# Kernel optimization log

Measured on AMD Instinct MI355X. Metric: run time of the kernel, lower is better.

The kernel has to match this reference:

```python
import jax, jax.numpy as jnp
import numpy as np

EPS = 1e-3       # module eps for mask normalization
LN_EPS = 1e-5    # torch LayerNorm default eps


def _layernorm(x, w, b):
    mu = jnp.mean(x, axis=-1, keepdims=True)
    var = jnp.var(x, axis=-1, keepdims=True)
    return (x - mu) * jax.lax.rsqrt(var + LN_EPS) * w + b


def setup_inputs() -> dict:
    key = jax.random.key(0)
    ks = jax.random.split(key, 8)
    N_seq, N_res, c_m, c_h, c_z = 256, 256, 256, 32, 128
    m = jax.random.normal(ks[0], (N_seq, N_res, c_m), jnp.float32)
    mask = jnp.ones((N_seq, N_res), jnp.float32)
    s_m = 1.0 / np.sqrt(c_m)
    ln_w = jnp.ones((c_m,), jnp.float32)
    ln_b = jnp.zeros((c_m,), jnp.float32)
    w1 = jax.random.normal(ks[1], (c_m, c_h), jnp.float32) * s_m
    b1 = jnp.zeros((c_h,), jnp.float32)
    w2 = jax.random.normal(ks[2], (c_m, c_h), jnp.float32) * s_m
    b2 = jnp.zeros((c_h,), jnp.float32)
    # linear_out has init='final' (zeros) in training; use small random so the
    # reference output / gradients are non-trivial for kernel testing.
    w_out = jax.random.normal(ks[3], (c_h * c_h, c_z), jnp.float32) * 0.02
    b_out = jnp.zeros((c_z,), jnp.float32)
    return {"m": m, "mask": mask, "ln_w": ln_w, "ln_b": ln_b,
            "w1": w1, "b1": b1, "w2": w2, "b2": b2,
            "w_out": w_out, "b_out": b_out}


def reference(m, mask, ln_w, ln_b, w1, b1, w2, b2, w_out, b_out):
    # m: [N_seq, N_res, c_m], mask: [N_seq, N_res]
    ln = _layernorm(m, ln_w, ln_b)
    mk = mask[..., None]                                 # [S, N, 1]
    a = (ln @ w1 + b1) * mk                              # [S, N, h]
    b = (ln @ w2 + b2) * mk                              # [S, N, h]
    a = jnp.swapaxes(a, -2, -3)                          # [N, S, h]
    b = jnp.swapaxes(b, -2, -3)                          # [N, S, h]
    # outer product mean over sequences: [N, N, h, h]
    outer = jnp.einsum('isc,jse->ijce', a, b)
    N = outer.shape[0]
    outer = outer.reshape(N, N, -1)                      # [N, N, h*h]
    out = outer @ w_out + b_out                          # [N, N, c_z]
    norm = jnp.einsum('si,sj->ij', mask, mask) + EPS     # [N, N]
    return out / norm[..., None]
```

## Files before the change

kernel.cpp:

```cpp
#include <hip/hip_runtime.h>
#include <hip/hip_bf16.h>
#include <stdint.h>

typedef __bf16 bf16x8 __attribute__((ext_vector_type(8)));
typedef float  f32x4  __attribute__((ext_vector_type(4)));
typedef __attribute__((address_space(1))) uint32_t u32_g;
typedef __attribute__((address_space(3))) uint32_t u32_l;
typedef unsigned short u16;
typedef u16 u16x4 __attribute__((ext_vector_type(4)));

__device__ __forceinline__ void gload16(const void* g, void* l) {
    __builtin_amdgcn_global_load_lds((u32_g*)g, (u32_l*)l, 16, 0, 0);
}

__device__ __forceinline__ u16 bf16bits(float v) {
    __bf16 h = (__bf16)v;
    return __builtin_bit_cast(u16, h);
}

__global__ __launch_bounds__(256) void k_prep(const float* __restrict__ w_out,
                                              const float* __restrict__ mask,
                                              const float* __restrict__ w1,
                                              const float* __restrict__ w2,
                                              u16* __restrict__ WT,
                                              u16* __restrict__ WcatT,
                                              float* __restrict__ normv) {
    __shared__ float mcol[256];
    const int b = blockIdx.x, t = threadIdx.x;
    if (b < 512) {
        int idx = b * 256 + t;
        int z = idx >> 10, kc = idx & 1023;
        int c = kc & 31, e = kc >> 5;
        WT[idx] = bf16bits(w_out[(c * 32 + e) * 128 + z]);
    } else if (b < 576) {
        int idx = (b - 512) * 256 + t;
        int n = idx >> 8, k = idx & 255;
        float v = (n < 32) ? w1[k * 32 + n] : w2[k * 32 + (n - 32)];
        WcatT[idx] = bf16bits(v);
    } else {
        int i = b - 576;
        mcol[t] = mask[(size_t)t * 256 + i];
        __syncthreads();
        float acc = 1e-3f;
#pragma unroll 8
        for (int s = 0; s < 256; ++s)
            acc += mcol[s] * mask[(size_t)s * 256 + t];
        normv[i * 256 + t] = acc;
    }
}

__global__ __launch_bounds__(256, 2) void k_lnproj(
        const float* __restrict__ M, const float* __restrict__ mask,
        const float* __restrict__ lnw, const float* __restrict__ lnb,
        const float* __restrict__ b1, const float* __restrict__ b2,
        const u16* __restrict__ WcatT,
        u16* __restrict__ AT, u16* __restrict__ BT) {
    __shared__ __align__(16) u16 sh[32768];
    const int tid = threadIdx.x, lane = tid & 63, w = tid >> 6;
    const int i = blockIdx.x, s0 = blockIdx.y * 64;

#pragma unroll
    for (int p = 0; p < 8; ++p) {
        int flat = p * 256 + tid;
        int r = flat >> 5, slot = flat & 31;
        int gs = slot ^ (r & 7);
        const char* src = (const char*)WcatT + (size_t)r * 512 + (size_t)gs * 16;
        char* dst = (char*)sh + 32768 + (size_t)(p * 256 + (tid & ~63)) * 16;
        gload16(src, dst);
    }

    float4 wv = *(const float4*)(lnw + lane * 4);
    float4 bv = *(const float4*)(lnb + lane * 4);
    float4 xv[16];
#pragma unroll
    for (int it = 0; it < 16; ++it) {
        int s = s0 + w * 16 + it;
        xv[it] = *(const float4*)(M + ((size_t)s * 256 + i) * 256 + lane * 4);
    }
#pragma unroll
    for (int it = 0; it < 16; ++it) {
        int row = w * 16 + it;
        float4 x = xv[it];
        float s1 = x.x + x.y + x.z + x.w;
        float s2 = x.x * x.x + x.y * x.y + x.z * x.z + x.w * x.w;
#pragma unroll
        for (int o = 1; o < 64; o <<= 1) {
            s1 += __shfl_xor(s1, o);
            s2 += __shfl_xor(s2, o);
        }
        float mu   = s1 * 0.00390625f;
        float var  = s2 * 0.00390625f - mu * mu;
        float rstd = rsqrtf(var + 1e-5f);
        u16x4 pk;
        pk[0] = bf16bits((x.x - mu) * rstd * wv.x + bv.x);
        pk[1] = bf16bits((x.y - mu) * rstd * wv.y + bv.y);
        pk[2] = bf16bits((x.z - mu) * rstd * wv.z + bv.z);
        pk[3] = bf16bits((x.w - mu) * rstd * wv.w + bv.w);
        int byte = (row * 512 + lane * 8) ^ ((row & 7) << 4);
        *(u16x4*)((char*)sh + byte) = pk;
    }
    __syncthreads();

    f32x4 acc[4] = {};
#pragma unroll
    for (int kk = 0; kk < 8; ++kk) {
        int kb = kk * 64 + ((lane >> 4) << 4);
        int arow = w * 16 + (lane & 15);
        bf16x8 af = *(const bf16x8*)((const char*)sh +
                     ((arow * 512 + kb) ^ ((arow & 7) << 4)));
#pragma unroll
        for (int f = 0; f < 4; ++f) {
            int nrow = f * 16 + (lane & 15);
            bf16x8 bfr = *(const bf16x8*)((const char*)sh + 32768 +
                          ((nrow * 512 + kb) ^ ((nrow & 7) << 4)));
            acc[f] = __builtin_amdgcn_mfma_f32_16x16x32_bf16(af, bfr, acc[f], 0, 0, 0);
        }
    }

    const int sb = s0 + w * 16 + ((lane >> 4) << 2);
    float mk[4];
#pragma unroll
    for (int r = 0; r < 4; ++r) mk[r] = mask[(size_t)(sb + r) * 256 + i];
#pragma unroll
    for (int f = 0; f < 4; ++f) {
        int col = f * 16 + (lane & 15);
        float bias = (col < 32) ? b1[col] : b2[col - 32];
        u16* dst = ((col < 32) ? AT : BT) + ((size_t)i * 32 + (col & 31)) * 256 + sb;
        u16x4 pk;
#pragma unroll
        for (int r = 0; r < 4; ++r)
            pk[r] = bf16bits((acc[f][r] + bias) * mk[r]);
        *(u16x4*)dst = pk;
    }
}

__global__ __launch_bounds__(512, 2) void k_fused(
        const u16* __restrict__ AT, const u16* __restrict__ BT,
        const u16* __restrict__ WT, const float* __restrict__ normv,
        const float* __restrict__ b_out, float* __restrict__ out) {
    __shared__ __align__(16) u16 sh[65536];
    const int tid  = threadIdx.x;
    const int lane = tid & 63;
    const int wid  = tid >> 6;
    const int wr   = wid >> 2, wc = wid & 3;
    const int lid = blockIdx.x;
    const int swz = (lid & 7) * 128 + (lid >> 3);
    const int bx = swz & 31, by = swz >> 5;
    const int m0 = bx * 256, n0 = by * 256;

    f32x4 acc[8][4] = {};

    auto stage = [&](int kt, int bufsel) {
        const int k0 = kt * 64;
        const size_t bb = (size_t)bufsel * 65536;
#pragma unroll
        for (int ii = 0; ii < 4; ++ii) {
            int f = ii * 512 + tid;
            int r = f >> 3, slot = f & 7;
            int gs = slot ^ (r & 7);
            gload16((const char*)AT + (((size_t)(m0 + r)) * 256 + k0) * 2 + gs * 16,
                    (char*)sh + bb + (size_t)(ii * 512 + (tid & ~63)) * 16);
        }
#pragma unroll
        for (int ii = 0; ii < 4; ++ii) {
            int f = ii * 512 + tid;
            int r = f >> 3, slot = f & 7;
            int gs = slot ^ (r & 7);
            gload16((const char*)BT + (((size_t)(n0 + r)) * 256 + k0) * 2 + gs * 16,
                    (char*)sh + bb + 32768 + (size_t)(ii * 512 + (tid & ~63)) * 16);
        }
    };

    auto compute = [&](int bufsel) {
        const char* Ab = (const char*)sh + (size_t)bufsel * 65536;
        const char* Bb = Ab + 32768;
#pragma unroll
        for (int ks = 0; ks < 2; ++ks) {
            bf16x8 af[8], bfr[4];
            const int kb = ks * 64 + ((lane >> 4) << 4);
#pragma unroll
            for (int f = 0; f < 8; ++f) {
                int row = wr * 128 + f * 16 + (lane & 15);
                af[f] = *(const bf16x8*)(Ab + row * 128 + (kb ^ ((row & 7) << 4)));
            }
#pragma unroll
            for (int f = 0; f < 4; ++f) {
                int row = wc * 64 + f * 16 + (lane & 15);
                bfr[f] = *(const bf16x8*)(Bb + row * 128 + (kb ^ ((row & 7) << 4)));
            }
#pragma unroll
            for (int mi = 0; mi < 8; ++mi)
#pragma unroll
                for (int nj = 0; nj < 4; ++nj)
                    acc[mi][nj] = __builtin_amdgcn_mfma_f32_16x16x32_bf16(
                        af[mi], bfr[nj], acc[mi][nj], 0, 0, 0);
        }
    };

    stage(0, 0);
#pragma unroll
    for (int kt = 0; kt < 4; ++kt) {
        __syncthreads();
        if (kt < 3) stage(kt + 1, (kt + 1) & 1);
        compute(kt & 1);
    }
    __syncthreads();

#pragma unroll
    for (int mi = 0; mi < 8; ++mi)
#pragma unroll
        for (int nj = 0; nj < 4; ++nj) {
            int m = wr * 128 + mi * 16 + ((lane >> 4) << 2);
            int n = wc * 64 + nj * 16 + (lane & 15);
            int pr = ((m >> 5) << 3) | (n >> 5);
            int c0 = m & 31, e = n & 31;
            int byte = pr * 2048 + (e * 32 + c0) * 2;
            byte ^= ((pr ^ e) & 7) << 4;
            u16x4 pk;
#pragma unroll
            for (int r = 0; r < 4; ++r)
                pk[r] = bf16bits(acc[mi][nj][r]);
            *(u16x4*)((char*)sh + byte) = pk;
        }
    __syncthreads();

    f32x4 acc2[2][2] = {};
    const int prb = wr * 32 + (lane & 15);
    const int zb  = wc * 32 + (lane & 15);
    const int ko  = (lane >> 4) << 3;
#pragma unroll 4
    for (int ks = 0; ks < 32; ++ks) {
        const int kc = ks * 32 + ko;
        bf16x8 pa[2], wb[2];
#pragma unroll
        for (int mf = 0; mf < 2; ++mf) {
            int pr = prb + mf * 16;
            int byte = pr * 2048 + kc * 2;
            byte ^= ((pr ^ ks) & 7) << 4;
            pa[mf] = *(const bf16x8*)((const char*)sh + byte);
        }
#pragma unroll
        for (int zf = 0; zf < 2; ++zf) {
            int z = zb + zf * 16;
            wb[zf] = *(const bf16x8*)(WT + (size_t)z * 1024 + kc);
        }
#pragma unroll
        for (int mf = 0; mf < 2; ++mf)
#pragma unroll
            for (int zf = 0; zf < 2; ++zf)
                acc2[mf][zf] = __builtin_amdgcn_mfma_f32_16x16x32_bf16(
                    pa[mf], wb[zf], acc2[mf][zf], 0, 0, 0);
    }

    const int i0 = bx * 8, j0 = by * 8;
#pragma unroll
    for (int mf = 0; mf < 2; ++mf)
#pragma unroll
        for (int zf = 0; zf < 2; ++zf)
#pragma unroll
            for (int r = 0; r < 4; ++r) {
                int pr = wr * 32 + mf * 16 + ((lane >> 4) << 2) + r;
                int z  = wc * 32 + zf * 16 + (lane & 15);
                int i = i0 + (pr >> 3), j = j0 + (pr & 7);
                float val = (acc2[mf][zf][r] + b_out[z]) / normv[i * 256 + j];
                out[((size_t)(i * 256 + j)) * 128 + z] = val;
            }
}

extern "C" void kernel_launch(void* const* d_in, const int* in_sizes, int n_in,
                              void* d_out, int out_size, void* d_ws, size_t ws_size,
                              hipStream_t stream) {
    const float* M    = (const float*)d_in[0];
    const float* mask = (const float*)d_in[1];
    const float* lnw  = (const float*)d_in[2];
    const float* lnb  = (const float*)d_in[3];
    const float* w1   = (const float*)d_in[4];
    const float* b1   = (const float*)d_in[5];
    const float* w2   = (const float*)d_in[6];
    const float* b2   = (const float*)d_in[7];
    const float* wout = (const float*)d_in[8];
    const float* bout = (const float*)d_in[9];
    float* out = (float*)d_out;

    char* ws = (char*)d_ws;
    u16*   AT    = (u16*)(ws);
    u16*   BT    = (u16*)(ws + 4194304);
    u16*   WT    = (u16*)(ws + 8388608);
    float* normv = (float*)(ws + 8650752);
    u16*   WcatT = (u16*)(ws + 8912896);

    k_prep  <<<832, 256, 0, stream>>>(wout, mask, w1, w2, WT, WcatT, normv);
    k_lnproj<<<dim3(256, 4), 256, 0, stream>>>(M, mask, lnw, lnb, b1, b2, WcatT, AT, BT);
    k_fused <<<1024, 512, 0, stream>>>(AT, BT, WT, normv, bout, out);
}
```

Baseline: 128.0 us.

## Split fused GEMM main loop into quadrant phases with fine-grained load/compute interleave

The first GEMM's K loop is restructured into four quadrant phases per K tile. Each phase issues a slice of the next tile's global-to-LDS loads, uses explicit vmcnt waits and barriers rather than __syncthreads, and raises wave priority around the MFMA blocks (a ping-pong style schedule). The warp tile layout changes so each wave covers two 64x32 halves. The second GEMM prefetches w_out fragments three steps ahead in a register ring buffer. This is meant to hide global load latency and overlap LDS reads with MFMA, at the cost of more barriers, higher register pressure, and fragile hand-counted waitcnt values.

```diff
diff --git a/kernel.cpp b/kernel.cpp
--- a/kernel.cpp
+++ b/kernel.cpp
@@ -17,6 +17,12 @@
     __bf16 h = (__bf16)v;
     return __builtin_bit_cast(u16, h);
 }
+
+#define WAITV(n) asm volatile("s_waitcnt vmcnt(" #n ")" ::: "memory")
+#define WAITLGKM0() do { asm volatile("s_waitcnt lgkmcnt(0)" ::: "memory"); \
+                         __builtin_amdgcn_sched_barrier(0); } while (0)
+#define BAR() do { __builtin_amdgcn_s_barrier(); \
+                   __builtin_amdgcn_sched_barrier(0); } while (0)
 
 __global__ __launch_bounds__(256) void k_prep(const float* __restrict__ w_out,
                                               const float* __restrict__ mask,
@@ -143,6 +149,8 @@
     const int lane = tid & 63;
     const int wid  = tid >> 6;
     const int wr   = wid >> 2, wc = wid & 3;
+    const int l15  = lane & 15;
+    const int kq   = (lane >> 4) << 4;
     const int lid = blockIdx.x;
     const int swz = (lid & 7) * 128 + (lid >> 3);
     const int bx = swz & 31, by = swz >> 5;
@@ -150,106 +158,140 @@
 
     f32x4 acc[8][4] = {};
 
-    auto stage = [&](int kt, int bufsel) {
+    auto unit = [&](int kt, int which) {
+        const int half = which & 1, isB = which >> 1;
+        char* base = (char*)sh + (kt & 1) * 65536 + isB * 32768 + half * 16384;
+        const u16* srcm = isB ? BT : AT;
+        const int row0 = (isB ? n0 : m0) + half * 128;
         const int k0 = kt * 64;
-        const size_t bb = (size_t)bufsel * 65536;
-#pragma unroll
-        for (int ii = 0; ii < 4; ++ii) {
-            int f = ii * 512 + tid;
-            int r = f >> 3, slot = f & 7;
+#pragma unroll
+        for (int q = 0; q < 2; ++q) {
+            int flat = q * 512 + tid;
+            int r = flat >> 3, slot = flat & 7;
             int gs = slot ^ (r & 7);
-            gload16((const char*)AT + (((size_t)(m0 + r)) * 256 + k0) * 2 + gs * 16,
-                    (char*)sh + bb + (size_t)(ii * 512 + (tid & ~63)) * 16);
-        }
-#pragma unroll
-        for (int ii = 0; ii < 4; ++ii) {
-            int f = ii * 512 + tid;
-            int r = f >> 3, slot = f & 7;
-            int gs = slot ^ (r & 7);
-            gload16((const char*)BT + (((size_t)(n0 + r)) * 256 + k0) * 2 + gs * 16,
-                    (char*)sh + bb + 32768 + (size_t)(ii * 512 + (tid & ~63)) * 16);
+            gload16((const char*)srcm + (((size_t)(row0 + r)) * 256 + k0) * 2 + gs * 16,
+                    base + (size_t)(q * 512 + (tid & ~63)) * 16);
         }
     };
 
-    auto compute = [&](int bufsel) {
-        const char* Ab = (const char*)sh + (size_t)bufsel * 65536;
-        const char* Bb = Ab + 32768;
-#pragma unroll
-        for (int ks = 0; ks < 2; ++ks) {
-            bf16x8 af[8], bfr[4];
-            const int kb = ks * 64 + ((lane >> 4) << 4);
-#pragma unroll
-            for (int f = 0; f < 8; ++f) {
-                int row = wr * 128 + f * 16 + (lane & 15);
-                af[f] = *(const bf16x8*)(Ab + row * 128 + (kb ^ ((row & 7) << 4)));
-            }
-#pragma unroll
-            for (int f = 0; f < 4; ++f) {
-                int row = wc * 64 + f * 16 + (lane & 15);
-                bfr[f] = *(const bf16x8*)(Bb + row * 128 + (kb ^ ((row & 7) << 4)));
-            }
-#pragma unroll
-            for (int mi = 0; mi < 8; ++mi)
-#pragma unroll
-                for (int nj = 0; nj < 4; ++nj)
-                    acc[mi][nj] = __builtin_amdgcn_mfma_f32_16x16x32_bf16(
-                        af[mi], bfr[nj], acc[mi][nj], 0, 0, 0);
-        }
-    };
-
-    stage(0, 0);
-#pragma unroll
-    for (int kt = 0; kt < 4; ++kt) {
-        __syncthreads();
-        if (kt < 3) stage(kt + 1, (kt + 1) & 1);
-        compute(kt & 1);
-    }
-    __syncthreads();
-
-#pragma unroll
-    for (int mi = 0; mi < 8; ++mi)
-#pragma unroll
-        for (int nj = 0; nj < 4; ++nj) {
-            int m = wr * 128 + mi * 16 + ((lane >> 4) << 2);
-            int n = wc * 64 + nj * 16 + (lane & 15);
-            int pr = ((m >> 5) << 3) | (n >> 5);
-            int c0 = m & 31, e = n & 31;
-            int byte = pr * 2048 + (e * 32 + c0) * 2;
-            byte ^= ((pr ^ e) & 7) << 4;
-            u16x4 pk;
-#pragma unroll
-            for (int r = 0; r < 4; ++r)
-                pk[r] = bf16bits(acc[mi][nj][r]);
-            *(u16x4*)((char*)sh + byte) = pk;
-        }
-    __syncthreads();
+#define PHASE(BUFC, MH, NH, STAGE_CODE, TAIL_CODE) do {                          \
+    bf16x8 af_[4][2], bf_[2][2];                                                 \
+    const char* Ab_ = (BUFC) + (MH) * 16384;                                     \
+    const char* Bb_ = (BUFC) + 32768 + (NH) * 16384;                             \
+    _Pragma("unroll") for (int mi = 0; mi < 4; ++mi)                             \
+    _Pragma("unroll") for (int ks = 0; ks < 2; ++ks) {                           \
+        int rA = wr * 64 + mi * 16 + l15;                                        \
+        int kb = ks * 64 + kq;                                                   \
+        af_[mi][ks] = *(const bf16x8*)(Ab_ + rA * 128 + (kb ^ ((rA & 7) << 4))); \
+    }                                                                            \
+    _Pragma("unroll") for (int nj = 0; nj < 2; ++nj)                             \
+    _Pragma("unroll") for (int ks = 0; ks < 2; ++ks) {                           \
+        int rB = wc * 32 + nj * 16 + l15;                                        \
+        int kb = ks * 64 + kq;                                                   \
+        bf_[nj][ks] = *(const bf16x8*)(Bb_ + rB * 128 + (kb ^ ((rB & 7) << 4))); \
+    }                                                                            \
+    STAGE_CODE;                                                                  \
+    BAR();                                                                       \
+    WAITLGKM0();                                                                 \
+    __builtin_amdgcn_s_setprio(1);                                               \
+    _Pragma("unroll") for (int mi = 0; mi < 4; ++mi)                             \
+    _Pragma("unroll") for (int nj = 0; nj < 2; ++nj)                             \
+    _Pragma("unroll") for (int ks = 0; ks < 2; ++ks)                             \
+        acc[(MH)*4+mi][(NH)*2+nj] = __builtin_amdgcn_mfma_f32_16x16x32_bf16(     \
+            af_[mi][ks], bf_[nj][ks], acc[(MH)*4+mi][(NH)*2+nj], 0, 0, 0);       \
+    __builtin_amdgcn_s_setprio(0);                                               \
+    TAIL_CODE;                                                                   \
+    BAR();                                                                       \
+} while (0)
+
+    unit(0, 0); unit(0, 1); unit(0, 2); unit(0, 3);
+    unit(1, 0); unit(1, 2);
+    WAITV(4);
+    BAR();
+
+    { const char* bufc = (const char*)sh;
+      PHASE(bufc, 0, 0, { unit(1, 1); unit(1, 3); }, {});
+      PHASE(bufc, 1, 0, {}, {});
+      PHASE(bufc, 0, 1, { unit(2, 2); }, {});
+      PHASE(bufc, 1, 1, { unit(2, 0); }, { WAITV(4); });
+    }
+    { const char* bufc = (const char*)sh + 65536;
+      PHASE(bufc, 0, 0, { unit(2, 1); unit(2, 3); }, {});
+      PHASE(bufc, 1, 0, {}, {});
+      PHASE(bufc, 0, 1, { unit(3, 2); }, {});
+      PHASE(bufc, 1, 1, { unit(3, 0); }, { WAITV(4); });
+    }
+    { const char* bufc = (const char*)sh;
+      PHASE(bufc, 0, 0, { unit(3, 1); unit(3, 3); }, {});
+      PHASE(bufc, 1, 0, {}, {});
+      PHASE(bufc, 0, 1, {}, {});
+      PHASE(bufc, 1, 1, {}, { WAITV(0); });
+    }
+    { const char* bufc = (const char*)sh + 65536;
+      PHASE(bufc, 0, 0, {}, {});
+      PHASE(bufc, 1, 0, {}, {});
+      PHASE(bufc, 0, 1, {}, {});
+      PHASE(bufc, 1, 1, {}, {});
+    }
+#undef PHASE
+
+#pragma unroll
+    for (int mh = 0; mh < 2; ++mh)
+#pragma unroll
+    for (int mi = 0; mi < 4; ++mi)
+#pragma unroll
+    for (int nh = 0; nh < 2; ++nh)
+#pragma unroll
+    for (int nj = 0; nj < 2; ++nj) {
+        int m = mh * 128 + wr * 64 + mi * 16 + ((lane >> 4) << 2);
+        int n = nh * 128 + wc * 32 + nj * 16 + l15;
+        int pr = ((m >> 5) << 3) | (n >> 5);
+        int c0 = m & 31, e = n & 31;
+        int byte = pr * 2048 + (e * 32 + c0) * 2;
+        byte ^= ((pr ^ e) & 7) << 4;
+        u16x4 pk;
+#pragma unroll
+        for (int r = 0; r < 4; ++r)
+            pk[r] = bf16bits(acc[mh * 4 + mi][nh * 2 + nj][r]);
+        *(u16x4*)((char*)sh + byte) = pk;
+    }
+    asm volatile("s_waitcnt lgkmcnt(0)" ::: "memory");
+    BAR();
 
     f32x4 acc2[2][2] = {};
-    const int prb = wr * 32 + (lane & 15);
-    const int zb  = wc * 32 + (lane & 15);
+    const int prb = wr * 32 + l15;
+    const int zb  = wc * 32 + l15;
     const int ko  = (lane >> 4) << 3;
-#pragma unroll 4
+    bf16x8 wb[4][2];
+#pragma unroll
+    for (int d = 0; d < 3; ++d)
+#pragma unroll
+        for (int zf = 0; zf < 2; ++zf)
+            wb[d][zf] = *(const bf16x8*)(WT + (size_t)(zb + zf * 16) * 1024 + d * 32 + ko);
+#pragma unroll
     for (int ks = 0; ks < 32; ++ks) {
-        const int kc = ks * 32 + ko;
-        bf16x8 pa[2], wb[2];
+        if (ks + 3 < 32) {
+#pragma unroll
+            for (int zf = 0; zf < 2; ++zf)
+                wb[(ks + 3) & 3][zf] = *(const bf16x8*)(WT +
+                    (size_t)(zb + zf * 16) * 1024 + (ks + 3) * 32 + ko);
+        }
+        bf16x8 pa[2];
 #pragma unroll
         for (int mf = 0; mf < 2; ++mf) {
             int pr = prb + mf * 16;
-            int byte = pr * 2048 + kc * 2;
+            int byte = pr * 2048 + (ks * 32 + ko) * 2;
             byte ^= ((pr ^ ks) & 7) << 4;
             pa[mf] = *(const bf16x8*)((const char*)sh + byte);
         }
-#pragma unroll
-        for (int zf = 0; zf < 2; ++zf) {
-            int z = zb + zf * 16;
-            wb[zf] = *(const bf16x8*)(WT + (size_t)z * 1024 + kc);
-        }
+        __builtin_amdgcn_s_setprio(1);
 #pragma unroll
         for (int mf = 0; mf < 2; ++mf)
 #pragma unroll
             for (int zf = 0; zf < 2; ++zf)
                 acc2[mf][zf] = __builtin_amdgcn_mfma_f32_16x16x32_bf16(
-                    pa[mf], wb[zf], acc2[mf][zf], 0, 0, 0);
+                    pa[mf], wb[ks & 3][zf], acc2[mf][zf], 0, 0, 0);
+        __builtin_amdgcn_s_setprio(0);
     }
 
     const int i0 = bx * 8, j0 = by * 8;
@@ -260,7 +302,7 @@
 #pragma unroll
             for (int r = 0; r < 4; ++r) {
                 int pr = wr * 32 + mf * 16 + ((lane >> 4) << 2) + r;
-                int z  = wc * 32 + zf * 16 + (lane & 15);
+                int z  = wc * 32 + zf * 16 + l15;
                 int i = i0 + (pr >> 3), j = j0 + (pr & 7);
                 float val = (acc2[mf][zf][r] + b_out[z]) / normv[i * 256 + j];
                 out[((size_t)(i * 256 + j)) * 128 + z] = val;
```

Measured after the change: 133.2 us. +4.1%, slower.

## Halve fused-kernel tile, raise occupancy, software-pipeline the projection GEMM

Applied to the files above, without the earlier changes.

Shrinks the fused kernel's outer-product tile from 256x256 to 128x256 with a 32-wide K step. This cuts LDS use so four blocks can fit per CU, and doubles the grid. The main loop now uses explicit vmcnt waits and raw barriers, plus s_setprio around the MFMA bursts. The second GEMM is rebuilt so each wave owns 16 output channels, with register-prefetched weight and LDS operands across iterations. The tradeoffs: the unswizzled A/B LDS layout may cause bank conflicts, and the outer product is re-read redundantly from LDS by every wave.

```diff
diff --git a/kernel.cpp b/kernel.cpp
--- a/kernel.cpp
+++ b/kernel.cpp
@@ -17,6 +17,10 @@
     __bf16 h = (__bf16)v;
     return __builtin_bit_cast(u16, h);
 }
+
+#define WAITV0() asm volatile("s_waitcnt vmcnt(0)" ::: "memory")
+#define BAR() do { __builtin_amdgcn_s_barrier(); \
+                   __builtin_amdgcn_sched_barrier(0); } while (0)
 
 __global__ __launch_bounds__(256) void k_prep(const float* __restrict__ w_out,
                                               const float* __restrict__ mask,
@@ -134,84 +138,79 @@
     }
 }
 
-__global__ __launch_bounds__(512, 2) void k_fused(
+__global__ __launch_bounds__(512, 4) void k_fused(
         const u16* __restrict__ AT, const u16* __restrict__ BT,
         const u16* __restrict__ WT, const float* __restrict__ normv,
         const float* __restrict__ b_out, float* __restrict__ out) {
-    __shared__ __align__(16) u16 sh[65536];
+    __shared__ __align__(16) u16 sh[32768];
     const int tid  = threadIdx.x;
     const int lane = tid & 63;
     const int wid  = tid >> 6;
     const int wr   = wid >> 2, wc = wid & 3;
+    const int l15  = lane & 15;
+    const int q16  = lane >> 4;
     const int lid = blockIdx.x;
-    const int swz = (lid & 7) * 128 + (lid >> 3);
-    const int bx = swz & 31, by = swz >> 5;
-    const int m0 = bx * 256, n0 = by * 256;
-
-    f32x4 acc[8][4] = {};
-
-    auto stage = [&](int kt, int bufsel) {
-        const int k0 = kt * 64;
-        const size_t bb = (size_t)bufsel * 65536;
-#pragma unroll
-        for (int ii = 0; ii < 4; ++ii) {
-            int f = ii * 512 + tid;
-            int r = f >> 3, slot = f & 7;
-            int gs = slot ^ (r & 7);
-            gload16((const char*)AT + (((size_t)(m0 + r)) * 256 + k0) * 2 + gs * 16,
-                    (char*)sh + bb + (size_t)(ii * 512 + (tid & ~63)) * 16);
-        }
-#pragma unroll
-        for (int ii = 0; ii < 4; ++ii) {
-            int f = ii * 512 + tid;
-            int r = f >> 3, slot = f & 7;
-            int gs = slot ^ (r & 7);
-            gload16((const char*)BT + (((size_t)(n0 + r)) * 256 + k0) * 2 + gs * 16,
-                    (char*)sh + bb + 32768 + (size_t)(ii * 512 + (tid & ~63)) * 16);
+    const int swz = (lid & 7) * 256 + (lid >> 3);
+    const int bx = swz & 63, by = swz >> 6;
+    const int m0 = bx * 128, n0 = by * 256;
+
+    f32x4 acc[4][4] = {};
+
+    auto stage = [&](int kt, int buf) {
+        char* base = (char*)sh + buf * 24576;
+        const int k0 = kt * 32;
+        gload16((const char*)AT + (((size_t)(m0 + (tid >> 2))) * 256 + k0) * 2 + (tid & 3) * 16,
+                base + (size_t)tid * 16);
+#pragma unroll
+        for (int q = 0; q < 2; ++q) {
+            int flat = q * 512 + tid;
+            int r = flat >> 2, slot = flat & 3;
+            gload16((const char*)BT + (((size_t)(n0 + r)) * 256 + k0) * 2 + slot * 16,
+                    base + 8192 + (size_t)(q * 512 + (tid & ~63)) * 16);
         }
     };
 
-    auto compute = [&](int bufsel) {
-        const char* Ab = (const char*)sh + (size_t)bufsel * 65536;
-        const char* Bb = Ab + 32768;
-#pragma unroll
-        for (int ks = 0; ks < 2; ++ks) {
-            bf16x8 af[8], bfr[4];
-            const int kb = ks * 64 + ((lane >> 4) << 4);
-#pragma unroll
-            for (int f = 0; f < 8; ++f) {
-                int row = wr * 128 + f * 16 + (lane & 15);
-                af[f] = *(const bf16x8*)(Ab + row * 128 + (kb ^ ((row & 7) << 4)));
-            }
-#pragma unroll
-            for (int f = 0; f < 4; ++f) {
-                int row = wc * 64 + f * 16 + (lane & 15);
-                bfr[f] = *(const bf16x8*)(Bb + row * 128 + (kb ^ ((row & 7) << 4)));
-            }
-#pragma unroll
-            for (int mi = 0; mi < 8; ++mi)
-#pragma unroll
-                for (int nj = 0; nj < 4; ++nj)
-                    acc[mi][nj] = __builtin_amdgcn_mfma_f32_16x16x32_bf16(
-                        af[mi], bfr[nj], acc[mi][nj], 0, 0, 0);
-        }
+    auto compute = [&](int buf) {
+        const char* Ab = (const char*)sh + buf * 24576;
+        const char* Bb = Ab + 8192;
+        bf16x8 af[4], bfr[4];
+#pragma unroll
+        for (int mi = 0; mi < 4; ++mi) {
+            int rA = wr * 64 + mi * 16 + l15;
+            af[mi] = *(const bf16x8*)(Ab + rA * 64 + q16 * 16);
+        }
+#pragma unroll
+        for (int nj = 0; nj < 4; ++nj) {
+            int rB = wc * 64 + nj * 16 + l15;
+            bfr[nj] = *(const bf16x8*)(Bb + rB * 64 + q16 * 16);
+        }
+        __builtin_amdgcn_s_setprio(1);
+#pragma unroll
+        for (int mi = 0; mi < 4; ++mi)
+#pragma unroll
+            for (int nj = 0; nj < 4; ++nj)
+                acc[mi][nj] = __builtin_amdgcn_mfma_f32_16x16x32_bf16(
+                    af[mi], bfr[nj], acc[mi][nj], 0, 0, 0);
+        __builtin_amdgcn_s_setprio(0);
     };
 
     stage(0, 0);
-#pragma unroll
-    for (int kt = 0; kt < 4; ++kt) {
-        __syncthreads();
-        if (kt < 3) stage(kt + 1, (kt + 1) & 1);
-        compute(kt & 1);
-    }
-    __syncthreads();
-
-#pragma unroll
-    for (int mi = 0; mi < 8; ++mi)
+    WAITV0();
+    BAR();
+#pragma unroll
+    for (int t = 0; t < 8; ++t) {
+        if (t < 7) stage(t + 1, (t + 1) & 1);
+        compute(t & 1);
+        if (t < 7) WAITV0();
+        BAR();
+    }
+
+#pragma unroll
+    for (int mi = 0; mi < 4; ++mi)
 #pragma unroll
         for (int nj = 0; nj < 4; ++nj) {
-            int m = wr * 128 + mi * 16 + ((lane >> 4) << 2);
-            int n = wc * 64 + nj * 16 + (lane & 15);
+            int m = wr * 64 + mi * 16 + (q16 << 2);
+            int n = wc * 64 + nj * 16 + l15;
             int pr = ((m >> 5) << 3) | (n >> 5);
             int c0 = m & 31, e = n & 31;
             int byte = pr * 2048 + (e * 32 + c0) * 2;
@@ -225,46 +224,51 @@
     __syncthreads();
 
     f32x4 acc2[2][2] = {};
-    const int prb = wr * 32 + (lane & 15);
-    const int zb  = wc * 32 + (lane & 15);
-    const int ko  = (lane >> 4) << 3;
-#pragma unroll 4
+    const int zb = wid * 16 + l15;
+    const int ko = q16 * 8;
+    bf16x8 wbr[4];
+    bf16x8 par[2][2];
+#pragma unroll
+    for (int d = 0; d < 3; ++d)
+        wbr[d] = *(const bf16x8*)(WT + (size_t)zb * 1024 + d * 32 + ko);
+#pragma unroll
+    for (int pf = 0; pf < 2; ++pf) {
+        int prw = pf * 16 + l15;
+        int byte = (prw * 2048 + ko * 2) ^ ((prw & 7) << 4);
+        par[0][pf] = *(const bf16x8*)((const char*)sh + byte);
+    }
+#pragma unroll
     for (int ks = 0; ks < 32; ++ks) {
-        const int kc = ks * 32 + ko;
-        bf16x8 pa[2], wb[2];
-#pragma unroll
-        for (int mf = 0; mf < 2; ++mf) {
-            int pr = prb + mf * 16;
-            int byte = pr * 2048 + kc * 2;
-            byte ^= ((pr ^ ks) & 7) << 4;
-            pa[mf] = *(const bf16x8*)((const char*)sh + byte);
-        }
-#pragma unroll
-        for (int zf = 0; zf < 2; ++zf) {
-            int z = zb + zf * 16;
-            wb[zf] = *(const bf16x8*)(WT + (size_t)z * 1024 + kc);
-        }
-#pragma unroll
-        for (int mf = 0; mf < 2; ++mf)
-#pragma unroll
-            for (int zf = 0; zf < 2; ++zf)
-                acc2[mf][zf] = __builtin_amdgcn_mfma_f32_16x16x32_bf16(
-                    pa[mf], wb[zf], acc2[mf][zf], 0, 0, 0);
-    }
-
-    const int i0 = bx * 8, j0 = by * 8;
-#pragma unroll
-    for (int mf = 0; mf < 2; ++mf)
-#pragma unroll
-        for (int zf = 0; zf < 2; ++zf)
-#pragma unroll
-            for (int r = 0; r < 4; ++r) {
-                int pr = wr * 32 + mf * 16 + ((lane >> 4) << 2) + r;
-                int z  = wc * 32 + zf * 16 + (lane & 15);
-                int i = i0 + (pr >> 3), j = j0 + (pr & 7);
-                float val = (acc2[mf][zf][r] + b_out[z]) / normv[i * 256 + j];
-                out[((size_t)(i * 256 + j)) * 128 + z] = val;
+        if (ks + 3 < 32)
+            wbr[(ks + 3) & 3] = *(const bf16x8*)(WT + (size_t)zb * 1024 + (ks + 3) * 32 + ko);
+        if (ks + 1 < 32) {
+#pragma unroll
+            for (int pf = 0; pf < 2; ++pf) {
+                int prw = pf * 16 + l15;
+                int byte = (prw * 2048 + ((ks + 1) * 32 + ko) * 2)
+                           ^ (((prw ^ (ks + 1)) & 7) << 4);
+                par[(ks + 1) & 1][pf] = *(const bf16x8*)((const char*)sh + byte);
             }
+        }
+        __builtin_amdgcn_s_setprio(1);
+#pragma unroll
+        for (int pf = 0; pf < 2; ++pf)
+            acc2[pf][ks & 1] = __builtin_amdgcn_mfma_f32_16x16x32_bf16(
+                par[ks & 1][pf], wbr[ks & 3], acc2[pf][ks & 1], 0, 0, 0);
+        __builtin_amdgcn_s_setprio(0);
+    }
+
+    const int i0 = bx * 4, j0 = by * 8;
+#pragma unroll
+    for (int pf = 0; pf < 2; ++pf)
+#pragma unroll
+        for (int r = 0; r < 4; ++r) {
+            int pr = pf * 16 + (q16 << 2) + r;
+            int z  = zb;
+            int i = i0 + (pr >> 3), j = j0 + (pr & 7);
+            float val = (acc2[pf][0][r] + acc2[pf][1][r] + b_out[z]) / normv[i * 256 + j];
+            out[((size_t)(i * 256 + j)) * 128 + z] = val;
+        }
 }
 
 extern "C" void kernel_launch(void* const* d_in, const int* in_sizes, int n_in,
@@ -291,5 +295,5 @@
 
     k_prep  <<<832, 256, 0, stream>>>(wout, mask, w1, w2, WT, WcatT, normv);
     k_lnproj<<<dim3(256, 4), 256, 0, stream>>>(M, mask, lnw, lnb, b1, b2, WcatT, AT, BT);
-    k_fused <<<1024, 512, 0, stream>>>(AT, BT, WT, normv, bout, out);
-}
+    k_fused <<<2048, 512, 0, stream>>>(AT, BT, WT, normv, bout, out);
+}
```

Result: faster. 121.0 us (-5.5%).
